# Optimization experiments

Measured on AMD Instinct MI355X. Metric: run time of the kernel, lower is better.

The kernel has to match this reference:

```python
import jax, jax.numpy as jnp
import numpy as np

B, N, M, D = 64, 16384, 64, 512
EPS = 1e-16


def setup_inputs() -> dict:
    key = jax.random.key(0)
    k1, k2, k3, k4 = jax.random.split(key, 4)
    controller_output = jax.random.normal(k1, (B, D), dtype=jnp.float32)
    w_prev = jax.random.uniform(k2, (B, N), dtype=jnp.float32)
    memory = jax.random.normal(k3, (B, N, M), dtype=jnp.float32)
    W = jax.random.normal(k4, (M + 6, D), dtype=jnp.float32) * (1.0 / np.sqrt(D))
    b = jnp.zeros((M + 6,), dtype=jnp.float32)
    return {"controller_output": controller_output, "w_prev": w_prev,
            "memory": memory, "W": W, "b": b}


def reference(controller_output, w_prev, memory, W, b):
    # fc_read projection -> [B, M+6], split into k, beta, g, s, gamma
    o = controller_output @ W.T + b
    k = o[:, :M]                      # [B, M] content key
    beta = jax.nn.softplus(o[:, M:M + 1])        # [B, 1] key strength
    g = jax.nn.sigmoid(o[:, M + 1:M + 2])        # [B, 1] interpolation gate
    s = jax.nn.softmax(o[:, M + 2:M + 5], axis=1)  # [B, 3] shift weights
    gamma = 1.0 + jax.nn.softplus(o[:, M + 5:M + 6])  # [B, 1] sharpening

    # content addressing: cosine similarity between k and each memory row
    num = jnp.einsum('bm,bnm->bn', k, memory)                      # [B, N]
    denom = (jnp.linalg.norm(k, axis=1, keepdims=True)
             * jnp.linalg.norm(memory, axis=2) + EPS)              # [B, N]
    w_c = jax.nn.softmax(beta * (num / denom), axis=1)             # [B, N]

    # interpolation with previous weighting
    w_g = g * w_c + (1.0 - g) * w_prev                              # [B, N]

    # circular convolution shift over {-1, 0, +1}
    w_t = (s[:, 0:1] * jnp.roll(w_g, 1, axis=1)
           + s[:, 1:2] * w_g
           + s[:, 2:3] * jnp.roll(w_g, -1, axis=1))                 # [B, N]

    # sharpening
    w_pow = w_t ** gamma
    w = w_pow / (jnp.sum(w_pow, axis=1, keepdims=True) + EPS)       # [B, N]

    # read: weighted sum of memory rows
    r = jnp.einsum('bn,bnm->bm', w, memory)                         # [B, M]
    return (r, w)
```

## Files before the change

### kernel.cpp

```cpp
#include <hip/hip_runtime.h>
#include <math.h>

#define B 64
#define N 16384
#define MDIM 64
#define DDIM 512
#define EPSF 1e-16f
#define NCH 32
#define CHUNK 512
#define GRID (B * NCH)

typedef float f4 __attribute__((ext_vector_type(4)));

#define K_OFF      0
#define SCAL_OFF   (B*64)
#define SCORE_OFF  (SCAL_OFF + B*8)
#define MS_OFF     (SCORE_OFF + B*N)
#define PSUM_OFF   (MS_OFF + B*NCH*2)
#define PART_OFF   (PSUM_OFF + B*NCH)

__device__ __forceinline__ float rowsum16(float x) {
    float t;
    t = __int_as_float(__builtin_amdgcn_update_dpp(0, __float_as_int(x), 0x128, 0xF, 0xF, true)); x += t;
    t = __int_as_float(__builtin_amdgcn_update_dpp(0, __float_as_int(x), 0x124, 0xF, 0xF, true)); x += t;
    t = __int_as_float(__builtin_amdgcn_update_dpp(0, __float_as_int(x), 0x122, 0xF, 0xF, true)); x += t;
    t = __int_as_float(__builtin_amdgcn_update_dpp(0, __float_as_int(x), 0x121, 0xF, 0xF, true)); x += t;
    return x;
}

__global__ __launch_bounds__(256) void k1(const float* __restrict__ c,
                                          const float* __restrict__ W,
                                          const float* __restrict__ bias,
                                          float* __restrict__ ws) {
    int b = blockIdx.x;
    __shared__ float cs[DDIM];
    __shared__ float osh[72];
    int tid = threadIdx.x;
    for (int i = tid; i < DDIM; i += 256) cs[i] = c[b * DDIM + i];
    __syncthreads();
    int wave = tid >> 6, lane = tid & 63;
    for (int j = wave; j < MDIM + 6; j += 4) {
        const float* wr = W + (size_t)j * DDIM;
        float sum = 0.f;
        for (int d = lane; d < DDIM; d += 64) sum += cs[d] * wr[d];
        for (int off = 32; off > 0; off >>= 1) sum += __shfl_xor(sum, off);
        if (lane == 0) osh[j] = sum + bias[j];
    }
    __syncthreads();
    if (tid < 64) ws[K_OFF + b * 64 + tid] = osh[tid];
    if (wave == 0) {
        float v = osh[lane];
        float sq = v * v;
        for (int off = 32; off > 0; off >>= 1) sq += __shfl_xor(sq, off);
        if (lane == 0) {
            float kn = sqrtf(sq);
            float ob = osh[64], og = osh[65], os0 = osh[66], os1 = osh[67],
                  os2 = osh[68], ogm = osh[69];
            float beta  = fmaxf(ob, 0.f) + log1pf(expf(-fabsf(ob)));
            float g     = 1.f / (1.f + expf(-og));
            float mx    = fmaxf(os0, fmaxf(os1, os2));
            float e0 = expf(os0 - mx), e1 = expf(os1 - mx), e2 = expf(os2 - mx);
            float es = e0 + e1 + e2;
            float gamma = 1.f + fmaxf(ogm, 0.f) + log1pf(expf(-fabsf(ogm)));
            float* sc = ws + SCAL_OFF + b * 8;
            sc[0] = kn; sc[1] = beta; sc[2] = g;
            sc[3] = e0 / es; sc[4] = e1 / es; sc[5] = e2 / es;
            sc[6] = gamma;
        }
    }
}

__global__ __launch_bounds__(256, 8) void k2(const float* __restrict__ mem,
                                             float* __restrict__ ws) {
    int b = blockIdx.x >> 5, chunk = blockIdx.x & 31;
    __shared__ float ks[64];
    __shared__ float kb2[2];
    __shared__ float scbuf[CHUNK];
    int tid = threadIdx.x;
    if (tid < 64) ks[tid] = ws[K_OFF + b * 64 + tid];
    if (tid == 64) kb2[0] = ws[SCAL_OFF + b * 8 + 0];
    if (tid == 65) kb2[1] = ws[SCAL_OFF + b * 8 + 1];
    __syncthreads();
    float kn = kb2[0], beta = kb2[1];
    int grp = tid >> 4, ll = tid & 15;
    float k0 = ks[ll * 4], k1v = ks[ll * 4 + 1], k2v = ks[ll * 4 + 2], k3v = ks[ll * 4 + 3];
    int row0 = chunk * CHUNK;
    #pragma unroll 8
    for (int it = 0; it < CHUNK / 16; ++it) {
        int lrow = it * 16 + grp;
        float4 v = *reinterpret_cast<const float4*>(
            mem + ((size_t)b * N + row0 + lrow) * MDIM + ll * 4);
        float dot = v.x * k0 + v.y * k1v + v.z * k2v + v.w * k3v;
        float sq  = v.x * v.x + v.y * v.y + v.z * v.z + v.w * v.w;
        dot = rowsum16(dot);
        sq  = rowsum16(sq);
        if (ll == 0)
            scbuf[lrow] = beta * (dot / (kn * sqrtf(sq) + EPSF));
    }
    __syncthreads();
    {
        float s0v = scbuf[tid], s1v = scbuf[tid + 256];
        float* sco = ws + SCORE_OFF + (size_t)b * N + row0;
        sco[tid] = s0v;
        sco[tid + 256] = s1v;
    }
    if (tid < 64) {
        float vr[8];
        float m = -1e30f;
        #pragma unroll
        for (int j = 0; j < 8; ++j) {
            vr[j] = scbuf[tid + 64 * j];
            m = fmaxf(m, vr[j]);
        }
        #pragma unroll
        for (int off = 32; off > 0; off >>= 1) m = fmaxf(m, __shfl_xor(m, off));
        float s = 0.f;
        #pragma unroll
        for (int j = 0; j < 8; ++j) s += __expf(vr[j] - m);
        #pragma unroll
        for (int off = 32; off > 0; off >>= 1) s += __shfl_xor(s, off);
        if (tid == 0) {
            ws[MS_OFF + ((size_t)b * NCH + chunk) * 2]     = m;
            ws[MS_OFF + ((size_t)b * NCH + chunk) * 2 + 1] = s;
        }
    }
}

__global__ __launch_bounds__(256, 8) void krw(const float* __restrict__ mem,
                                              const float* __restrict__ w_prev,
                                              float* __restrict__ ws,
                                              float* __restrict__ w_out,
                                              float* __restrict__ part) {
    int b = blockIdx.x >> 5, chunk = blockIdx.x & 31;
    int tid = threadIdx.x, wave = tid >> 6, lane = tid & 63;
    int grp = tid >> 4, ll = tid & 15;
    __shared__ float wgL[CHUNK + 2];
    __shared__ float wpl[CHUNK];
    __shared__ float lds[16][64];
    __shared__ float red[4];
    int row0 = chunk * CHUNK;

    const f4* mbase = (const f4*)(mem + ((size_t)b * N + row0 + grp) * MDIM + ll * 4);
    f4 pre[4];
    #pragma unroll
    for (int j = 0; j < 4; ++j)
        pre[j] = __builtin_nontemporal_load(mbase + j * 256);

    const float* sl = ws + SCAL_OFF + b * 8;
    float g = sl[2], s0 = sl[3], s1 = sl[4], s2 = sl[5], gamma = sl[6];

    const float* msp = ws + MS_OFF + (size_t)b * NCH * 2;
    float mi = -1e30f, si = 0.f;
    if (lane < NCH) {
        mi = msp[lane * 2];
        si = msp[lane * 2 + 1];
    }
    #pragma unroll
    for (int off = 32; off > 0; off >>= 1) {
        float m2 = __shfl_xor(mi, off), s2x = __shfl_xor(si, off);
        float M = fmaxf(mi, m2);
        si = si * __expf(mi - M) + s2x * __expf(m2 - M);
        mi = M;
    }
    float mx = mi;
    float inv = 1.f / si;

    const float* sc = ws + SCORE_OFF + (size_t)b * N;
    const float* wp = w_prev + (size_t)b * N;

    {
        int r0 = row0 + tid;
        wgL[tid + 1]   = g * (__expf(sc[r0] - mx) * inv) + (1.f - g) * wp[r0];
        int r1 = row0 + tid + 256;
        wgL[tid + 257] = g * (__expf(sc[r1] - mx) * inv) + (1.f - g) * wp[r1];
        if (tid == 0) {
            int rl = (row0 - 1) & (N - 1);
            wgL[0] = g * (__expf(sc[rl] - mx) * inv) + (1.f - g) * wp[rl];
        }
        if (tid == 255) {
            int rr = (row0 + CHUNK) & (N - 1);
            wgL[CHUNK + 1] = g * (__expf(sc[rr] - mx) * inv) + (1.f - g) * wp[rr];
        }
    }
    __syncthreads();

    float wt0 = s0 * wgL[tid]       + s1 * wgL[tid + 1]   + s2 * wgL[tid + 2];
    float wt1 = s0 * wgL[tid + 256] + s1 * wgL[tid + 257] + s2 * wgL[tid + 258];
    float p0 = __expf(gamma * __logf(wt0));
    float p1 = __expf(gamma * __logf(wt1));
    wpl[tid] = p0;
    wpl[tid + 256] = p1;
    float* wo = w_out + (size_t)b * N + row0;
    wo[tid]       = p0;
    wo[tid + 256] = p1;

    float sp = p0 + p1;
    #pragma unroll
    for (int off = 32; off > 0; off >>= 1) sp += __shfl_xor(sp, off);
    if (lane == 0) red[wave] = sp;
    __syncthreads();
    if (tid == 0)
        ws[PSUM_OFF + (size_t)b * NCH + chunk] = red[0] + red[1] + red[2] + red[3];

    f4 acc = (f4)(0.f);
    #pragma unroll
    for (int it = 0; it < CHUNK / 16; ++it) {
        f4 v = pre[it & 3];
        int nxt = it + 4;
        if (nxt < CHUNK / 16)
            pre[it & 3] = __builtin_nontemporal_load(mbase + nxt * 256);
        float wv = wpl[it * 16 + grp];
        acc += wv * v;
    }
    lds[grp][ll * 4 + 0] = acc.x;
    lds[grp][ll * 4 + 1] = acc.y;
    lds[grp][ll * 4 + 2] = acc.z;
    lds[grp][ll * 4 + 3] = acc.w;
    __syncthreads();
    if (tid < 64) {
        float sacc = 0.f;
        #pragma unroll
        for (int gi = 0; gi < 16; ++gi) sacc += lds[gi][tid];
        part[(size_t)blockIdx.x * 64 + tid] = sacc;
    }
}

__global__ __launch_bounds__(256) void kfin(const float* __restrict__ part,
                                            float* __restrict__ ws,
                                            float* __restrict__ w_out,
                                            float* __restrict__ r) {
    int b = blockIdx.x >> 5, chunk = blockIdx.x & 31;
    int tid = threadIdx.x;
    __shared__ float invps;
    if (tid < 64) {
        float s = (tid < 32) ? ws[PSUM_OFF + (size_t)b * NCH + tid] : 0.f;
        #pragma unroll
        for (int off = 32; off > 0; off >>= 1) s += __shfl_xor(s, off);
        if (tid == 0) invps = 1.f / (s + EPSF);
    }
    __syncthreads();
    float invp = invps;
    size_t base = (size_t)b * N + chunk * CHUNK;
    w_out[base + tid]       *= invp;
    w_out[base + tid + 256] *= invp;
    if (chunk == 0 && tid < 64) {
        float srr = 0.f;
        #pragma unroll
        for (int c2 = 0; c2 < NCH; ++c2)
            srr += part[((size_t)b * NCH + c2) * 64 + tid];
        r[b * 64 + tid] = srr * invp;
    }
}

extern "C" void kernel_launch(void* const* d_in, const int* in_sizes, int n_in,
                              void* d_out, int out_size, void* d_ws, size_t ws_size,
                              hipStream_t stream) {
    const float* c      = (const float*)d_in[0];
    const float* w_prev = (const float*)d_in[1];
    const float* mem    = (const float*)d_in[2];
    const float* W      = (const float*)d_in[3];
    const float* bias   = (const float*)d_in[4];
    float* out = (float*)d_out;
    float* r_out = out;
    float* w_out = out + B * MDIM;
    float* ws = (float*)d_ws;
    float* part = ws + PART_OFF;

    k1  <<<B,    256, 0, stream>>>(c, W, bias, ws);
    k2  <<<GRID, 256, 0, stream>>>(mem, ws);
    krw <<<GRID, 256, 0, stream>>>(mem, w_prev, ws, w_out, part);
    kfin<<<GRID, 256, 0, stream>>>(part, ws, w_out, r_out);
}
```

Before: 109.0 us.

## Pipeline batch groups so krw re-reads memory from cache after k2

Splits the batch into four groups of 16 and launches mixed kernels in which k2 scoring for group i+1 runs alongside krw for group i. The memory slice for a group is then read a second time soon after the first pass, while it may still be in the L2 or last-level cache. The krw memory loads switch from nontemporal to normal loads so those lines can stay cached. The cost is extra kernel launches, smaller grids per launch, and heterogeneous blocks inside one kernel.

```diff
diff --git a/kernel.cpp b/kernel.cpp
--- a/kernel.cpp
+++ b/kernel.cpp
@@ -8,6 +8,9 @@
 #define EPSF 1e-16f
 #define NCH 32
 #define CHUNK 512
+#define GB 16
+#define NG (B / GB)
+#define GBLK (GB * NCH)
 #define GRID (B * NCH)
 
 typedef float f4 __attribute__((ext_vector_type(4)));
@@ -70,9 +73,9 @@
     }
 }
 
-__global__ __launch_bounds__(256, 8) void k2(const float* __restrict__ mem,
-                                             float* __restrict__ ws) {
-    int b = blockIdx.x >> 5, chunk = blockIdx.x & 31;
+__device__ __forceinline__ void k2_body(int b, int chunk,
+                                        const float* __restrict__ mem,
+                                        float* __restrict__ ws) {
     __shared__ float ks[64];
     __shared__ float kb2[2];
     __shared__ float scbuf[CHUNK];
@@ -126,12 +129,12 @@
     }
 }
 
-__global__ __launch_bounds__(256, 8) void krw(const float* __restrict__ mem,
-                                              const float* __restrict__ w_prev,
-                                              float* __restrict__ ws,
-                                              float* __restrict__ w_out,
-                                              float* __restrict__ part) {
-    int b = blockIdx.x >> 5, chunk = blockIdx.x & 31;
+__device__ __forceinline__ void krw_body(int b, int chunk,
+                                         const float* __restrict__ mem,
+                                         const float* __restrict__ w_prev,
+                                         float* __restrict__ ws,
+                                         float* __restrict__ w_out,
+                                         float* __restrict__ part) {
     int tid = threadIdx.x, wave = tid >> 6, lane = tid & 63;
     int grp = tid >> 4, ll = tid & 15;
     __shared__ float wgL[CHUNK + 2];
@@ -143,8 +146,7 @@
     const f4* mbase = (const f4*)(mem + ((size_t)b * N + row0 + grp) * MDIM + ll * 4);
     f4 pre[4];
     #pragma unroll
-    for (int j = 0; j < 4; ++j)
-        pre[j] = __builtin_nontemporal_load(mbase + j * 256);
+    for (int j = 0; j < 4; ++j) pre[j] = mbase[j * 256];
 
     const float* sl = ws + SCAL_OFF + b * 8;
     float g = sl[2], s0 = sl[3], s1 = sl[4], s2 = sl[5], gamma = sl[6];
@@ -207,8 +209,7 @@
     for (int it = 0; it < CHUNK / 16; ++it) {
         f4 v = pre[it & 3];
         int nxt = it + 4;
-        if (nxt < CHUNK / 16)
-            pre[it & 3] = __builtin_nontemporal_load(mbase + nxt * 256);
+        if (nxt < CHUNK / 16) pre[it & 3] = mbase[nxt * 256];
         float wv = wpl[it * 16 + grp];
         acc += wv * v;
     }
@@ -221,7 +222,35 @@
         float sacc = 0.f;
         #pragma unroll
         for (int gi = 0; gi < 16; ++gi) sacc += lds[gi][tid];
-        part[(size_t)blockIdx.x * 64 + tid] = sacc;
+        part[((size_t)b * NCH + chunk) * 64 + tid] = sacc;
+    }
+}
+
+__global__ __launch_bounds__(256, 8) void k2k(const float* __restrict__ mem,
+                                              float* __restrict__ ws, int b0) {
+    k2_body(b0 + (blockIdx.x >> 5), blockIdx.x & 31, mem, ws);
+}
+
+__global__ __launch_bounds__(256, 8) void krwk(const float* __restrict__ mem,
+                                               const float* __restrict__ w_prev,
+                                               float* __restrict__ ws,
+                                               float* __restrict__ w_out,
+                                               float* __restrict__ part, int b0) {
+    krw_body(b0 + (blockIdx.x >> 5), blockIdx.x & 31, mem, w_prev, ws, w_out, part);
+}
+
+__global__ __launch_bounds__(256, 8) void kmix(const float* __restrict__ mem,
+                                               const float* __restrict__ w_prev,
+                                               float* __restrict__ ws,
+                                               float* __restrict__ w_out,
+                                               float* __restrict__ part,
+                                               int k2_b0, int krw_b0) {
+    int bid = blockIdx.x;
+    if (bid < GBLK) {
+        k2_body(k2_b0 + (bid >> 5), bid & 31, mem, ws);
+    } else {
+        bid -= GBLK;
+        krw_body(krw_b0 + (bid >> 5), bid & 31, mem, w_prev, ws, w_out, part);
     }
 }
 
@@ -266,8 +295,11 @@
     float* ws = (float*)d_ws;
     float* part = ws + PART_OFF;
 
-    k1  <<<B,    256, 0, stream>>>(c, W, bias, ws);
-    k2  <<<GRID, 256, 0, stream>>>(mem, ws);
-    krw <<<GRID, 256, 0, stream>>>(mem, w_prev, ws, w_out, part);
-    kfin<<<GRID, 256, 0, stream>>>(part, ws, w_out, r_out);
-}
+    k1  <<<B,        256, 0, stream>>>(c, W, bias, ws);
+    k2k <<<GBLK,     256, 0, stream>>>(mem, ws, 0);
+    kmix<<<2 * GBLK, 256, 0, stream>>>(mem, w_prev, ws, w_out, part, GB,     0);
+    kmix<<<2 * GBLK, 256, 0, stream>>>(mem, w_prev, ws, w_out, part, 2 * GB, GB);
+    kmix<<<2 * GBLK, 256, 0, stream>>>(mem, w_prev, ws, w_out, part, 3 * GB, 2 * GB);
+    krwk<<<GBLK,     256, 0, stream>>>(mem, w_prev, ws, w_out, part, 3 * GB);
+    kfin<<<GRID,     256, 0, stream>>>(part, ws, w_out, r_out);
+}
```

After: 142.7 us. 1.31x slower.
